# Optimization experiments

Measured on AMD Instinct MI355X. Metric: run time of the kernel, lower is better.

## Reference

```python
import jax, jax.numpy as jnp
import numpy as np

# FP4 E2M1 lookup table: low 3 bits = magnitude code, bit 3 = sign
E2M1_LUT = jnp.array([0.0, 0.5, 1.0, 1.5, 2.0, 3.0, 4.0, 6.0,
                      -0.0, -0.5, -1.0, -1.5, -2.0, -3.0, -4.0, -6.0],
                     dtype=jnp.float32)

INNER_BLOCK = 16    # elements per fp8 (e4m3) inner scale
OUTER_BLOCK = 128   # elements per fp32 outlier scale


def dequant_fp4(w_q, w_os, w_is):
    """Dequantize packed FP4 weights.
    w_q : [out, in//2] int (uint8 semantics: two nibbles per byte)
    w_os: [out, in//128] fp32 outlier scales
    w_is: [out, in//16]  fp32 values on the fp8 e4m3 grid (inner scales)
    returns W: [out, in] fp32
    """
    out_f = w_q.shape[0]
    lo = E2M1_LUT[w_q & 0xF]          # even in-feature indices
    hi = E2M1_LUT[(w_q >> 4) & 0xF]   # odd in-feature indices
    w = jnp.stack([lo, hi], axis=-1).reshape(out_f, -1)  # [out, in]
    w = w * jnp.repeat(w_is, INNER_BLOCK, axis=1)
    w = w * jnp.repeat(w_os, OUTER_BLOCK, axis=1)
    return w


def setup_inputs() -> dict:
    key = jax.random.key(0)
    k1, k2, k3, k4 = jax.random.split(key, 4)
    M, IN, OUT = 8192, 4096, 16384

    x = jax.random.normal(k1, (M, IN), dtype=jnp.float32)

    # packed FP4 codes (uint8 semantics, stored as int32 for portability)
    w_q = jax.random.randint(k2, (OUT, IN // 2), 0, 256, dtype=jnp.int32)

    # per-128-block fp32 outlier scales (positive)
    w_os = jax.random.uniform(k3, (OUT, IN // OUTER_BLOCK), dtype=jnp.float32,
                              minval=0.001, maxval=0.01)

    # per-16-block inner scales, snapped to the fp8 e4m3 grid
    w_is_raw = jax.random.uniform(k4, (OUT, IN // INNER_BLOCK), dtype=jnp.float32,
                                  minval=0.25, maxval=2.0)
    w_is = w_is_raw.astype(jnp.float8_e4m3fn).astype(jnp.float32)

    # transposed dequantized weight, exactly consistent (used by backward)
    w_t = dequant_fp4(w_q, w_os, w_is).T  # [IN, OUT]

    return {"x": x, "w_q": w_q, "w_os": w_os, "w_is": w_is, "w_t": w_t}


def reference(x, w_q, w_os, w_is, w_t):
    # x.float() + flatten-to-2D already satisfied by setup (x is [M, in] fp32).
    w = dequant_fp4(w_q, w_os, w_is)          # [out, in]
    y = jnp.einsum('mk,nk->mn', x, w)         # fused dequant + GEMM math
    return y
```

## Files before the change

kernel.cpp:

```cpp
#include <hip/hip_runtime.h>
#include <hip/hip_bf16.h>
#include <stdint.h>
#include <stddef.h>

#define M_DIM 8192
#define K_DIM 4096
#define N_DIM 16384

#define BM 256
#define BN 256
#define BK 32
#define KSTEPS (K_DIM / BK)
#define SLOT_SH (BM * BK)
#define NSLOT 4

typedef __attribute__((ext_vector_type(8))) short bf16x8;
typedef __attribute__((ext_vector_type(4))) float f32x4;
typedef __attribute__((ext_vector_type(4))) int   i32x4;

static __device__ __forceinline__ short f2bf(float f) {
    union { float f; uint32_t u; } v; v.f = f;
    uint32_t r = v.u + 0x7FFFu + ((v.u >> 16) & 1u);
    return (short)(r >> 16);
}

static __device__ __forceinline__ float e2m1(int v) {
    int e = (v >> 1) & 3;
    int m = v & 1;
    float mag = (e == 0) ? 0.5f * (float)m
                         : (float)(2 + m) * 0.25f * (float)(1 << e);
    return (v & 8) ? -mag : mag;
}

static __device__ __forceinline__ void gload16(short* lds, const short* g) {
    __builtin_amdgcn_global_load_lds(
        (const __attribute__((address_space(1))) void*)g,
        (__attribute__((address_space(3))) void*)lds,
        16, 0, 0);
}

__global__ void cast_x_kernel(const float* __restrict__ x, short* __restrict__ xb) {
    size_t i = (size_t)blockIdx.x * 256 + threadIdx.x;
    const float4* s = reinterpret_cast<const float4*>(x);
    float4 a = s[2 * i];
    float4 b = s[2 * i + 1];
    bf16x8 o;
    o[0] = f2bf(a.x); o[1] = f2bf(a.y); o[2] = f2bf(a.z); o[3] = f2bf(a.w);
    o[4] = f2bf(b.x); o[5] = f2bf(b.y); o[6] = f2bf(b.z); o[7] = f2bf(b.w);
    reinterpret_cast<bf16x8*>(xb)[i] = o;
}

__global__ void dequant_w_kernel(const int* __restrict__ wq,
                                 const float* __restrict__ wos,
                                 const float* __restrict__ wis,
                                 short* __restrict__ wb) {
    int tid = blockIdx.x * 256 + threadIdx.x;
    int n   = tid >> 8;
    int blk = tid & 255;
    float scale = wis[(n << 8) | blk] * wos[(n << 5) | (blk >> 3)];
    const i32x4* q = reinterpret_cast<const i32x4*>(wq + ((size_t)n << 11) + (blk << 3));
    i32x4 q0 = q[0], q1 = q[1];
    bf16x8 o0, o1;
#pragma unroll
    for (int j = 0; j < 4; ++j) {
        int c = q0[j];
        o0[2 * j]     = f2bf(e2m1(c & 15) * scale);
        o0[2 * j + 1] = f2bf(e2m1((c >> 4) & 15) * scale);
    }
#pragma unroll
    for (int j = 0; j < 4; ++j) {
        int c = q1[j];
        o1[2 * j]     = f2bf(e2m1(c & 15) * scale);
        o1[2 * j + 1] = f2bf(e2m1((c >> 4) & 15) * scale);
    }
    bf16x8* dst = reinterpret_cast<bf16x8*>(wb) + 2 * (size_t)tid;
    dst[0] = o0;
    dst[1] = o1;
}

__global__ __launch_bounds__(512)
void gemm_bt_kernel(const short* __restrict__ A,
                    const short* __restrict__ B,
                    float* __restrict__ C) {
    __shared__ __align__(16) short As[NSLOT * SLOT_SH];
    __shared__ __align__(16) short Bs[NSLOT * SLOT_SH];

    int bid = blockIdx.x;
    int xcd = bid & 7;
    int idx = bid >> 3;
    int im  = idx >> 3;
    int in8 = idx & 7;
    int bm  = im << 8;
    int bn  = ((xcd << 3) + in8) << 8;

    int t    = threadIdx.x;
    int lane = t & 63;
    int w    = t >> 6;
    int wm   = w >> 2;
    int wn   = w & 3;
    int fr   = lane & 15;
    int fq   = lane >> 4;
    int wbase = w << 9;

    int gcol = (((t & 3) ^ ((t >> 3) & 3)) << 3);
    const short* AgB = A + (size_t)(bm + (t >> 2)) * K_DIM + gcol;
    const short* BgB = B + (size_t)(bn + (t >> 2)) * K_DIM + gcol;

    int slot = fq ^ ((fr >> 1) & 3);
    int aoff[8], boff[4];
#pragma unroll
    for (int mi = 0; mi < 8; ++mi)
        aoff[mi] = ((wm << 7) + mi * 16 + fr) * 4 + slot;
#pragma unroll
    for (int ni = 0; ni < 4; ++ni)
        boff[ni] = ((wn << 6) + ni * 16 + fr) * 4 + slot;

    f32x4 acc[8][4] = {};

#define STAGE_A(slot_, kt_)                                                   \
    do {                                                                      \
        const short* _s = AgB + (size_t)(kt_) * BK;                           \
        short* _d = As + (slot_) * SLOT_SH + wbase;                           \
        gload16(_d,        _s);                                               \
        gload16(_d + 4096, _s + (size_t)128 * K_DIM);                         \
    } while (0)
#define STAGE_B(slot_, kt_)                                                   \
    do {                                                                      \
        const short* _s = BgB + (size_t)(kt_) * BK;                           \
        short* _d = Bs + (slot_) * SLOT_SH + wbase;                           \
        gload16(_d,        _s);                                               \
        gload16(_d + 4096, _s + (size_t)128 * K_DIM);                         \
    } while (0)

    bf16x8 aP[8], bP[4], aQ[8], bQ[4];

    STAGE_A(0, 0); STAGE_B(0, 0);
    STAGE_A(1, 1); STAGE_B(1, 1);
    STAGE_A(2, 2); STAGE_B(2, 2);
    asm volatile("s_waitcnt vmcnt(4)" ::: "memory");
    __builtin_amdgcn_s_barrier();
    {
        const bf16x8* Af = reinterpret_cast<const bf16x8*>(As);
        const bf16x8* Bf = reinterpret_cast<const bf16x8*>(Bs);
#pragma unroll
        for (int ni = 0; ni < 4; ++ni) bP[ni] = Bf[boff[ni]];
#pragma unroll
        for (int mi = 0; mi < 8; ++mi) aP[mi] = Af[aoff[mi]];
    }

#define TILE(tt, aC, bC, aN, bN)                                              \
    do {                                                                      \
        int ktn  = ((tt) + 3) & (KSTEPS - 1);          \
        int sStg = ((tt) + 3) & 3;                                            \
        const bf16x8* AfN = reinterpret_cast<const bf16x8*>(As + (((tt) + 1) & 3) * SLOT_SH); \
        const bf16x8* BfN = reinterpret_cast<const bf16x8*>(Bs + (((tt) + 1) & 3) * SLOT_SH); \
        STAGE_A(sStg, ktn);                                                   \
        _Pragma("unroll")                                                     \
        for (int ni = 0; ni < 4; ++ni) bN[ni] = BfN[boff[ni]];                \
        _Pragma("unroll")                                                     \
        for (int mi = 0; mi < 4; ++mi) aN[mi] = AfN[aoff[mi]];                \
        __builtin_amdgcn_sched_barrier(0);                                    \
        __builtin_amdgcn_s_setprio(1);                                        \
        _Pragma("unroll")                                                     \
        for (int mi = 0; mi < 4; ++mi)                                        \
            _Pragma("unroll")                                                 \
            for (int ni = 0; ni < 4; ++ni)                                    \
                acc[mi][ni] = __builtin_amdgcn_mfma_f32_16x16x32_bf16(        \
                    aC[mi], bC[ni], acc[mi][ni], 0, 0, 0);                    \
        __builtin_amdgcn_s_setprio(0);                                        \
        __builtin_amdgcn_sched_barrier(0);                                    \
        STAGE_B(sStg, ktn);                                                   \
        _Pragma("unroll")                                                     \
        for (int mi = 4; mi < 8; ++mi) aN[mi] = AfN[aoff[mi]];                \
        __builtin_amdgcn_sched_barrier(0);                                    \
        __builtin_amdgcn_s_setprio(1);                                        \
        _Pragma("unroll")                                                     \
        for (int mi = 4; mi < 8; ++mi)                                        \
            _Pragma("unroll")                                                 \
            for (int ni = 0; ni < 4; ++ni)                                    \
                acc[mi][ni] = __builtin_amdgcn_mfma_f32_16x16x32_bf16(        \
                    aC[mi], bC[ni], acc[mi][ni], 0, 0, 0);                    \
        __builtin_amdgcn_s_setprio(0);                                        \
        \
        \
        asm volatile("s_waitcnt vmcnt(4)" ::: "memory");                      \
        __builtin_amdgcn_s_barrier();                                         \
        __builtin_amdgcn_sched_barrier(0);                                    \
    } while (0)

    for (int tt = 0; tt < KSTEPS; tt += 2) {
        TILE(tt,     aP, bP, aQ, bQ);
        TILE(tt + 1, aQ, bQ, aP, bP);
    }
#undef TILE
#undef STAGE_A
#undef STAGE_B

#pragma unroll
    for (int mi = 0; mi < 8; ++mi) {
#pragma unroll
        for (int j = 0; j < 4; ++j) {
            size_t row = (size_t)(bm + (wm << 7) + mi * 16 + fq * 4 + j);
            float* Crow = C + row * N_DIM + (bn + (wn << 6) + fr);
#pragma unroll
            for (int ni = 0; ni < 4; ++ni)
                Crow[ni * 16] = acc[mi][ni][j];
        }
    }
}

extern "C" void kernel_launch(void* const* d_in, const int* in_sizes, int n_in,
                              void* d_out, int out_size, void* d_ws, size_t ws_size,
                              hipStream_t stream) {
    const float* x   = (const float*)d_in[0];
    const int*   wq  = (const int*)d_in[1];
    const float* wos = (const float*)d_in[2];
    const float* wis = (const float*)d_in[3];
    float* out = (float*)d_out;

    short* xb = (short*)d_ws;
    short* wb = (short*)((char*)d_ws + (size_t)M_DIM * K_DIM * 2);

    cast_x_kernel<<<(M_DIM * (size_t)K_DIM / 8) / 256, 256, 0, stream>>>(x, xb);
    dequant_w_kernel<<<(N_DIM * (size_t)K_DIM / 16) / 256, 256, 0, stream>>>(wq, wos, wis, wb);
    gemm_bt_kernel<<<(M_DIM / BM) * (N_DIM / BN), 512, 0, stream>>>(xb, wb, out);
}
```

Measured before the change: 1.163 ms.

## Stagger wave schedules so half the waves issue MFMA while others load

Splits the waves of the block into two groups with different phase orderings. Waves 0-3 issue global staging and LDS reads first, then MFMAs. Waves 4-7 start with MFMAs and do their loads afterwards. The aim is to interleave memory and matrix-core work across waves within each barrier interval, reducing contention where all waves hit LDS or MFMA at the same time. This adds a divergent wave-level branch and relies on `w` being the wave index, with 8 waves per block.

```diff
diff --git a/kernel.cpp b/kernel.cpp
--- a/kernel.cpp
+++ b/kernel.cpp
@@ -132,6 +132,84 @@
         gload16(_d + 4096, _s + (size_t)128 * K_DIM);                         \
     } while (0)
 
+#define FILL_LO(aN, bN, AfN, BfN)                                             \
+    do {                                                                      \
+        _Pragma("unroll")                                                     \
+        for (int ni = 0; ni < 4; ++ni) bN[ni] = BfN[boff[ni]];                \
+        _Pragma("unroll")                                                     \
+        for (int mi = 0; mi < 4; ++mi) aN[mi] = AfN[aoff[mi]];                \
+    } while (0)
+#define FILL_HI(aN, AfN)                                                      \
+    do {                                                                      \
+        _Pragma("unroll")                                                     \
+        for (int mi = 4; mi < 8; ++mi) aN[mi] = AfN[aoff[mi]];                \
+    } while (0)
+#define MFMA_LO(aC, bC)                                                       \
+    do {                                                                      \
+        __builtin_amdgcn_s_setprio(1);                                        \
+        _Pragma("unroll")                                                     \
+        for (int mi = 0; mi < 4; ++mi)                                        \
+            _Pragma("unroll")                                                 \
+            for (int ni = 0; ni < 4; ++ni)                                    \
+                acc[mi][ni] = __builtin_amdgcn_mfma_f32_16x16x32_bf16(        \
+                    aC[mi], bC[ni], acc[mi][ni], 0, 0, 0);                    \
+        __builtin_amdgcn_s_setprio(0);                                        \
+    } while (0)
+#define MFMA_HI(aC, bC)                                                       \
+    do {                                                                      \
+        __builtin_amdgcn_s_setprio(1);                                        \
+        _Pragma("unroll")                                                     \
+        for (int mi = 4; mi < 8; ++mi)                                        \
+            _Pragma("unroll")                                                 \
+            for (int ni = 0; ni < 4; ++ni)                                    \
+                acc[mi][ni] = __builtin_amdgcn_mfma_f32_16x16x32_bf16(        \
+                    aC[mi], bC[ni], acc[mi][ni], 0, 0, 0);                    \
+        __builtin_amdgcn_s_setprio(0);                                        \
+    } while (0)
+#define SB() __builtin_amdgcn_sched_barrier(0)
+#define BOUNDARY()                                                            \
+    do {                                                                      \
+        asm volatile("s_waitcnt vmcnt(4)" ::: "memory");                      \
+        __builtin_amdgcn_s_barrier();                                         \
+        SB();                                                                 \
+    } while (0)
+
+#define TILE_RD(tt, aC, bC, aN, bN)                                           \
+    do {                                                                      \
+        int ktn  = ((tt) + 3) & (KSTEPS - 1);                                 \
+        int sStg = ((tt) + 3) & 3;                                            \
+        const bf16x8* AfN = reinterpret_cast<const bf16x8*>(As + (((tt) + 1) & 3) * SLOT_SH); \
+        const bf16x8* BfN = reinterpret_cast<const bf16x8*>(Bs + (((tt) + 1) & 3) * SLOT_SH); \
+        STAGE_A(sStg, ktn);                                                   \
+        FILL_LO(aN, bN, AfN, BfN);                                            \
+        SB();                                                                 \
+        MFMA_LO(aC, bC);                                                      \
+        SB();                                                                 \
+        STAGE_B(sStg, ktn);                                                   \
+        FILL_HI(aN, AfN);                                                     \
+        SB();                                                                 \
+        MFMA_HI(aC, bC);                                                      \
+        BOUNDARY();                                                           \
+    } while (0)
+
+#define TILE_MF(tt, aC, bC, aN, bN)                                           \
+    do {                                                                      \
+        int ktn  = ((tt) + 3) & (KSTEPS - 1);                                 \
+        int sStg = ((tt) + 3) & 3;                                            \
+        const bf16x8* AfN = reinterpret_cast<const bf16x8*>(As + (((tt) + 1) & 3) * SLOT_SH); \
+        const bf16x8* BfN = reinterpret_cast<const bf16x8*>(Bs + (((tt) + 1) & 3) * SLOT_SH); \
+        MFMA_LO(aC, bC);                                                      \
+        SB();                                                                 \
+        STAGE_A(sStg, ktn);                                                   \
+        FILL_LO(aN, bN, AfN, BfN);                                            \
+        SB();                                                                 \
+        MFMA_HI(aC, bC);                                                      \
+        SB();                                                                 \
+        STAGE_B(sStg, ktn);                                                   \
+        FILL_HI(aN, AfN);                                                     \
+        BOUNDARY();                                                           \
+    } while (0)
+
     bf16x8 aP[8], bP[4], aQ[8], bQ[4];
 
     STAGE_A(0, 0); STAGE_B(0, 0);
@@ -148,51 +226,25 @@
         for (int mi = 0; mi < 8; ++mi) aP[mi] = Af[aoff[mi]];
     }
 
-#define TILE(tt, aC, bC, aN, bN)                                              \
-    do {                                                                      \
-        int ktn  = ((tt) + 3) & (KSTEPS - 1);          \
-        int sStg = ((tt) + 3) & 3;                                            \
-        const bf16x8* AfN = reinterpret_cast<const bf16x8*>(As + (((tt) + 1) & 3) * SLOT_SH); \
-        const bf16x8* BfN = reinterpret_cast<const bf16x8*>(Bs + (((tt) + 1) & 3) * SLOT_SH); \
-        STAGE_A(sStg, ktn);                                                   \
-        _Pragma("unroll")                                                     \
-        for (int ni = 0; ni < 4; ++ni) bN[ni] = BfN[boff[ni]];                \
-        _Pragma("unroll")                                                     \
-        for (int mi = 0; mi < 4; ++mi) aN[mi] = AfN[aoff[mi]];                \
-        __builtin_amdgcn_sched_barrier(0);                                    \
-        __builtin_amdgcn_s_setprio(1);                                        \
-        _Pragma("unroll")                                                     \
-        for (int mi = 0; mi < 4; ++mi)                                        \
-            _Pragma("unroll")                                                 \
-            for (int ni = 0; ni < 4; ++ni)                                    \
-                acc[mi][ni] = __builtin_amdgcn_mfma_f32_16x16x32_bf16(        \
-                    aC[mi], bC[ni], acc[mi][ni], 0, 0, 0);                    \
-        __builtin_amdgcn_s_setprio(0);                                        \
-        __builtin_amdgcn_sched_barrier(0);                                    \
-        STAGE_B(sStg, ktn);                                                   \
-        _Pragma("unroll")                                                     \
-        for (int mi = 4; mi < 8; ++mi) aN[mi] = AfN[aoff[mi]];                \
-        __builtin_amdgcn_sched_barrier(0);                                    \
-        __builtin_amdgcn_s_setprio(1);                                        \
-        _Pragma("unroll")                                                     \
-        for (int mi = 4; mi < 8; ++mi)                                        \
-            _Pragma("unroll")                                                 \
-            for (int ni = 0; ni < 4; ++ni)                                    \
-                acc[mi][ni] = __builtin_amdgcn_mfma_f32_16x16x32_bf16(        \
-                    aC[mi], bC[ni], acc[mi][ni], 0, 0, 0);                    \
-        __builtin_amdgcn_s_setprio(0);                                        \
-        \
-        \
-        asm volatile("s_waitcnt vmcnt(4)" ::: "memory");                      \
-        __builtin_amdgcn_s_barrier();                                         \
-        __builtin_amdgcn_sched_barrier(0);                                    \
-    } while (0)
-
-    for (int tt = 0; tt < KSTEPS; tt += 2) {
-        TILE(tt,     aP, bP, aQ, bQ);
-        TILE(tt + 1, aQ, bQ, aP, bP);
-    }
-#undef TILE
+    if (w < 4) {
+        for (int tt = 0; tt < KSTEPS; tt += 2) {
+            TILE_RD(tt,     aP, bP, aQ, bQ);
+            TILE_RD(tt + 1, aQ, bQ, aP, bP);
+        }
+    } else {
+        for (int tt = 0; tt < KSTEPS; tt += 2) {
+            TILE_MF(tt,     aP, bP, aQ, bQ);
+            TILE_MF(tt + 1, aQ, bQ, aP, bP);
+        }
+    }
+#undef TILE_RD
+#undef TILE_MF
+#undef BOUNDARY
+#undef SB
+#undef MFMA_LO
+#undef MFMA_HI
+#undef FILL_LO
+#undef FILL_HI
 #undef STAGE_A
 #undef STAGE_B
 
```

Measured after the change: 1.068 ms. 8.1% less time.
